# Kernel tuning notes

Measured on AMD Instinct MI355X. Metric: run time of the kernel, lower is better.

Reference implementation:

```python
import jax, jax.numpy as jnp
import numpy as np

N = 16777216
C = 2
BINS = 10
MOMENTUM = 0.75


def setup_inputs() -> dict:
    key = jax.random.key(0)
    k1, k2 = jax.random.split(key)
    outputs = jax.random.normal(k1, (N, C), dtype=jnp.float32)
    targets = jax.random.randint(k2, (N,), 0, C, dtype=jnp.int64)
    acc_sum = jnp.zeros((BINS,), dtype=jnp.float32)
    return {"outputs": outputs, "targets": targets, "acc_sum": acc_sum}


def reference(outputs, targets, acc_sum):
    n, c = outputs.shape
    tgt = targets.astype(jnp.int32)
    logp = jax.nn.log_softmax(outputs, axis=1)            # [N, C]
    p_t = jnp.take_along_axis(jnp.exp(logp), tgt[:, None], axis=1)[:, 0]
    # |softmax - onehot| summed over classes == 2 * (1 - p_target)
    g = 2.0 * (1.0 - p_t)                                 # [N], in [0, 2]
    # torch loop covers edges linspace(0,1,bins+1): only g in [0, 1) gets a weight
    bin_idx = jnp.clip(jnp.floor(g * BINS).astype(jnp.int32), 0, BINS - 1)
    valid = g < 1.0
    counts = jax.ops.segment_sum(jnp.where(valid, 1.0, 0.0).astype(jnp.float32),
                                 bin_idx, num_segments=BINS)  # [BINS]
    # acc_sum updated only for non-empty bins (EMA with momentum)
    new_acc = jnp.where(counts > 0, MOMENTUM * acc_sum + (1.0 - MOMENTUM) * counts, acc_sum)
    per_sample_acc = new_acc[bin_idx]
    weights = jnp.where(valid & (counts[bin_idx] > 0),
                        jnp.float32(n) / per_sample_acc,
                        jnp.float32(0.0))                 # [N]
    # cross_entropy(reduction='none') = -log_softmax[target]
    loss = -jnp.take_along_axis(logp, tgt[:, None], axis=1)[:, 0]
    return jnp.mean(loss * weights)
```

## Files before the change

kernel.cpp:

```cpp
#include <hip/hip_runtime.h>

#define BINS   10
#define ROWS   11
#define CSHIFT 26
#define QMASK  0x03FFFFFFu
#define QSCALE 2097152.0f


__global__ void ghm_zero_ws(unsigned* ws) {
    if (threadIdx.x < 32) ws[threadIdx.x] = 0u;
}

__device__ __forceinline__ void proc1(float o0, float o1, int t,
                                      unsigned (*h)[256], int tid) {
    float s  = o0 - o1;
    float d  = __int_as_float(__float_as_int(s) ^ (t << 31));
    float em = __expf(-d);
    float onep = 1.0f + em;
    float r  = __builtin_amdgcn_rcpf(onep);
    int bin  = (int)(20.0f * em * r);
    bin = min(bin, BINS - 1);
    bin = (d > 0.0f) ? bin : BINS;
    float loss = __logf(onep);
    unsigned q = (unsigned)(fmaf(loss, QSCALE, 0.5f));
    atomicAdd(&h[bin][tid], (1u << CSHIFT) + q);
}

__device__ __forceinline__ void proc4(float4 a, float4 b, int4 t,
                                      unsigned (*h)[256], int tid) {
    proc1(a.x, a.y, t.x, h, tid);
    proc1(a.z, a.w, t.y, h, tid);
    proc1(b.x, b.y, t.z, h, tid);
    proc1(b.z, b.w, t.w, h, tid);
}

__global__ __launch_bounds__(256, 4)
void ghm_main(const float* __restrict__ outs,
              const int*   __restrict__ tgt,
              float*       __restrict__ ws_lsum,
              unsigned*    __restrict__ ws_cnt,
              int n) {
    __shared__ unsigned h[ROWS][256];
    __shared__ unsigned s_c[BINS][16];
    __shared__ float    s_q[BINS][16];

    const int tid = threadIdx.x;
    #pragma unroll
    for (int r2 = 0; r2 < ROWS; ++r2) h[r2][tid] = 0u;
    __syncthreads();

    const int gid      = blockIdx.x * blockDim.x + tid;
    const int nthreads = gridDim.x * blockDim.x;
    const int npacks   = n >> 2;

    const float4* outs4 = (const float4*)outs;
    const int4*   tgt4  = (const int4*)tgt;

    int p = gid;
    for (; p + nthreads < npacks; p += 2 * nthreads) {
        int p2 = p + nthreads;
        float4 a0 = outs4[2 * p];
        float4 a1 = outs4[2 * p + 1];
        int4   t0 = tgt4[p];
        float4 b0 = outs4[2 * p2];
        float4 b1 = outs4[2 * p2 + 1];
        int4   t1 = tgt4[p2];
        proc4(a0, a1, t0, h, tid);
        proc4(b0, b1, t1, h, tid);
    }
    for (; p < npacks; p += nthreads) {
        float4 a0 = outs4[2 * p];
        float4 a1 = outs4[2 * p + 1];
        int4   t0 = tgt4[p];
        proc4(a0, a1, t0, h, tid);
    }
    int tail = n & 3;
    if (gid < tail) {
        int s = (npacks << 2) + gid;
        proc1(outs[2 * s], outs[2 * s + 1], tgt[s], h, tid);
    }
    __syncthreads();

    if (tid < 16 * BINS) {
        int bin  = tid >> 4;
        int part = tid & 15;
        unsigned c = 0, qs = 0;
        #pragma unroll
        for (int j = 0; j < 16; ++j) {
            unsigned v = h[bin][j * 16 + part];
            c  += v >> CSHIFT;
            qs += v & QMASK;
        }
        s_c[bin][part] = c;
        s_q[bin][part] = (float)qs;
    }
    __syncthreads();
    if (tid < BINS) {
        unsigned c = 0; float q = 0.0f;
        #pragma unroll
        for (int j = 0; j < 16; ++j) { c += s_c[tid][j]; q += s_q[tid][j]; }
        if (c) {
            atomicAdd(&ws_cnt[tid],  c);
            atomicAdd(&ws_lsum[tid], q * (1.0f / QSCALE));
        }
    }
}

__global__ void ghm_final(const float*    __restrict__ ws_lsum,
                          const unsigned* __restrict__ ws_cnt,
                          const float*    __restrict__ acc_sum,
                          float* __restrict__ out) {
    if (threadIdx.x == 0) {
        float r = 0.0f;
        #pragma unroll
        for (int b = 0; b < BINS; ++b) {
            unsigned c = ws_cnt[b];
            if (c > 0u) {
                float na = 0.75f * acc_sum[b] + 0.25f * (float)c;
                r += ws_lsum[b] / na;
            }
        }
        *out = r;
    }
}

extern "C" void kernel_launch(void* const* d_in, const int* in_sizes, int n_in,
                              void* d_out, int out_size, void* d_ws, size_t ws_size,
                              hipStream_t stream) {
    const float* outputs = (const float*)d_in[0];
    const int*   targets = (const int*)d_in[1];
    const float* acc_sum = (const float*)d_in[2];
    int n = in_sizes[1];

    float*    ws_lsum = (float*)d_ws;
    unsigned* ws_cnt  = (unsigned*)((char*)d_ws + 64);

    ghm_zero_ws<<<1, 64, 0, stream>>>((unsigned*)d_ws);
    ghm_main<<<2048, 256, 0, stream>>>(outputs, targets, ws_lsum, ws_cnt, n);
    ghm_final<<<1, 64, 0, stream>>>(ws_lsum, ws_cnt, acc_sum, (float*)d_out);
}
```

Measured before the change: 241.7 us.

## Replace LDS atomic histogram with register cumulative threshold bins

Each sample no longer does an LDS atomicAdd into a per-thread histogram slot. It compares its margin against precomputed logit thresholds and adds the packed count-plus-loss value into ten register accumulators, which build cumulative bins. The final kernel recovers per-bin values by differencing adjacent cumulative entries. This removes the reciprocal, the bin computation and the LDS atomics, and uses log2 with a scaled constant in place of log. The cost is ten compare-and-add operations per sample and more register pressure. Cumulative packed sums also risk overflowing the 26-bit quantized loss field and the 6-bit count field, since low bins now hold more samples per thread.

```diff
diff --git a/kernel.cpp b/kernel.cpp
--- a/kernel.cpp
+++ b/kernel.cpp
@@ -1,54 +1,49 @@
 #include <hip/hip_runtime.h>
 
 #define BINS   10
-#define ROWS   11
 #define CSHIFT 26
 #define QMASK  0x03FFFFFFu
 #define QSCALE 2097152.0f
+#define QLN2   1453635.25f
 
 
 __global__ void ghm_zero_ws(unsigned* ws) {
     if (threadIdx.x < 32) ws[threadIdx.x] = 0u;
 }
 
-__device__ __forceinline__ void proc1(float o0, float o1, int t,
-                                      unsigned (*h)[256], int tid) {
-    float s  = o0 - o1;
-    float d  = __int_as_float(__float_as_int(s) ^ (t << 31));
-    float em = __expf(-d);
+__device__ __forceinline__ void proc1(float o0, float o1, int t, unsigned* A) {
+    const float Th[BINS] = {
+        2.9444390f, 2.1972246f, 1.7346011f, 1.3862944f, 1.0986123f,
+        0.8472979f, 0.6190392f, 0.4054651f, 0.2006707f, 0.0f };
+    float s = o0 - o1;
+    float d = __int_as_float(__float_as_int(s) ^ (t << 31));
+    float em   = __expf(-d);
     float onep = 1.0f + em;
-    float r  = __builtin_amdgcn_rcpf(onep);
-    int bin  = (int)(20.0f * em * r);
-    bin = min(bin, BINS - 1);
-    bin = (d > 0.0f) ? bin : BINS;
-    float loss = __logf(onep);
-    unsigned q = (unsigned)(fmaf(loss, QSCALE, 0.5f));
-    atomicAdd(&h[bin][tid], (1u << CSHIFT) + q);
+    float qf   = fmaf(__log2f(onep), QLN2, 0.5f);
+    unsigned val = (unsigned)qf + (1u << CSHIFT);
+    #pragma unroll
+    for (int b = 0; b < BINS; ++b)
+        A[b] += (d > Th[b]) ? val : 0u;
 }
 
-__device__ __forceinline__ void proc4(float4 a, float4 b, int4 t,
-                                      unsigned (*h)[256], int tid) {
-    proc1(a.x, a.y, t.x, h, tid);
-    proc1(a.z, a.w, t.y, h, tid);
-    proc1(b.x, b.y, t.z, h, tid);
-    proc1(b.z, b.w, t.w, h, tid);
+__device__ __forceinline__ void proc4(float4 a, float4 b, int4 t, unsigned* A) {
+    proc1(a.x, a.y, t.x, A);
+    proc1(a.z, a.w, t.y, A);
+    proc1(b.x, b.y, t.z, A);
+    proc1(b.z, b.w, t.w, A);
 }
 
 __global__ __launch_bounds__(256, 4)
 void ghm_main(const float* __restrict__ outs,
               const int*   __restrict__ tgt,
-              float*       __restrict__ ws_lsum,
-              unsigned*    __restrict__ ws_cnt,
+              float*       __restrict__ ws_q,
+              unsigned*    __restrict__ ws_c,
               int n) {
-    __shared__ unsigned h[ROWS][256];
-    __shared__ unsigned s_c[BINS][16];
-    __shared__ float    s_q[BINS][16];
+    unsigned A[BINS];
+    #pragma unroll
+    for (int b = 0; b < BINS; ++b) A[b] = 0u;
 
-    const int tid = threadIdx.x;
-    #pragma unroll
-    for (int r2 = 0; r2 < ROWS; ++r2) h[r2][tid] = 0u;
-    __syncthreads();
-
+    const int tid      = threadIdx.x;
     const int gid      = blockIdx.x * blockDim.x + tid;
     const int nthreads = gridDim.x * blockDim.x;
     const int npacks   = n >> 2;
@@ -65,34 +60,40 @@
         float4 b0 = outs4[2 * p2];
         float4 b1 = outs4[2 * p2 + 1];
         int4   t1 = tgt4[p2];
-        proc4(a0, a1, t0, h, tid);
-        proc4(b0, b1, t1, h, tid);
+        proc4(a0, a1, t0, A);
+        proc4(b0, b1, t1, A);
     }
     for (; p < npacks; p += nthreads) {
         float4 a0 = outs4[2 * p];
         float4 a1 = outs4[2 * p + 1];
         int4   t0 = tgt4[p];
-        proc4(a0, a1, t0, h, tid);
+        proc4(a0, a1, t0, A);
     }
     int tail = n & 3;
     if (gid < tail) {
         int s = (npacks << 2) + gid;
-        proc1(outs[2 * s], outs[2 * s + 1], tgt[s], h, tid);
+        proc1(outs[2 * s], outs[2 * s + 1], tgt[s], A);
     }
+
+    __shared__ unsigned h[BINS][256];
+    __shared__ unsigned s_c[BINS][16];
+    __shared__ float    s_q[BINS][16];
+    #pragma unroll
+    for (int b = 0; b < BINS; ++b) h[b][tid] = A[b];
     __syncthreads();
 
     if (tid < 16 * BINS) {
         int bin  = tid >> 4;
         int part = tid & 15;
-        unsigned c = 0, qs = 0;
+        unsigned c = 0, q = 0;
         #pragma unroll
         for (int j = 0; j < 16; ++j) {
             unsigned v = h[bin][j * 16 + part];
-            c  += v >> CSHIFT;
-            qs += v & QMASK;
+            c += v >> CSHIFT;
+            q += v & QMASK;
         }
         s_c[bin][part] = c;
-        s_q[bin][part] = (float)qs;
+        s_q[bin][part] = (float)q;
     }
     __syncthreads();
     if (tid < BINS) {
@@ -100,24 +101,30 @@
         #pragma unroll
         for (int j = 0; j < 16; ++j) { c += s_c[tid][j]; q += s_q[tid][j]; }
         if (c) {
-            atomicAdd(&ws_cnt[tid],  c);
-            atomicAdd(&ws_lsum[tid], q * (1.0f / QSCALE));
+            atomicAdd(&ws_c[tid], c);
+            atomicAdd(&ws_q[tid], q * (1.0f / QSCALE));
         }
     }
 }
 
-__global__ void ghm_final(const float*    __restrict__ ws_lsum,
-                          const unsigned* __restrict__ ws_cnt,
+__global__ void ghm_final(const float*    __restrict__ ws_q,
+                          const unsigned* __restrict__ ws_c,
                           const float*    __restrict__ acc_sum,
                           float* __restrict__ out) {
     if (threadIdx.x == 0) {
         float r = 0.0f;
+        float    pq = 0.0f;
+        unsigned pc = 0u;
         #pragma unroll
         for (int b = 0; b < BINS; ++b) {
-            unsigned c = ws_cnt[b];
-            if (c > 0u) {
-                float na = 0.75f * acc_sum[b] + 0.25f * (float)c;
-                r += ws_lsum[b] / na;
+            float    cq = ws_q[b];
+            unsigned cc = ws_c[b];
+            unsigned cnt = cc - pc;
+            float    qs  = cq - pq;
+            pc = cc; pq = cq;
+            if (cnt > 0u) {
+                float na = 0.75f * acc_sum[b] + 0.25f * (float)cnt;
+                r += qs / na;
             }
         }
         *out = r;
@@ -132,10 +139,10 @@
     const float* acc_sum = (const float*)d_in[2];
     int n = in_sizes[1];
 
-    float*    ws_lsum = (float*)d_ws;
-    unsigned* ws_cnt  = (unsigned*)((char*)d_ws + 64);
+    float*    ws_q = (float*)d_ws;
+    unsigned* ws_c = (unsigned*)((char*)d_ws + 64);
 
     ghm_zero_ws<<<1, 64, 0, stream>>>((unsigned*)d_ws);
-    ghm_main<<<2048, 256, 0, stream>>>(outputs, targets, ws_lsum, ws_cnt, n);
-    ghm_final<<<1, 64, 0, stream>>>(ws_lsum, ws_cnt, acc_sum, (float*)d_out);
+    ghm_main<<<2048, 256, 0, stream>>>(outputs, targets, ws_q, ws_c, n);
+    ghm_final<<<1, 64, 0, stream>>>(ws_q, ws_c, acc_sum, (float*)d_out);
 }
```

Result: no change. 242.5 us (+0.3%).
